# Performance work log

Measured on AMD Instinct MI355X. Metric: run time of the kernel, lower is better.

## Reference

```python
import jax, jax.numpy as jnp
import numpy as np

B, L, C, H = 2, 2048, 1024, 16
D = C // H  # dim per head

def setup_inputs() -> dict:
    key = jax.random.key(0)
    ks = jax.random.split(key, 13)
    s = 1.0 / np.sqrt(C)
    inp = {
        "query": jax.random.normal(ks[0], (B, L, C), jnp.float32),
        "key": jax.random.normal(ks[1], (B, L, C), jnp.float32),
        "value": jax.random.normal(ks[2], (B, L, C), jnp.float32),
        "mask": jax.random.randint(ks[3], (B, 1, L, L), 0, 2, jnp.int32),
        "WQ": jax.random.normal(ks[4], (C, C), jnp.float32) * s,
        "bQ": jnp.zeros((C,), jnp.float32),
        "WK": jax.random.normal(ks[5], (C, C), jnp.float32) * s,
        "bK": jnp.zeros((C,), jnp.float32),
        "WV": jax.random.normal(ks[6], (C, C), jnp.float32) * s,
        "bV": jnp.zeros((C,), jnp.float32),
        "WO": jax.random.normal(ks[7], (C, C), jnp.float32) * s,
        "bO": jnp.zeros((C,), jnp.float32),
    }
    return inp

def reference(query, key, value, mask, WQ, bQ, WK, bK, WV, bV, WO, bO):
    b = query.shape[0]
    # projections: x @ W + b  (W stored [in, out])
    Q = query @ WQ + bQ
    K = key @ WK + bK
    V = value @ WV + bV
    # [B, L, C] -> [B, H, L, D]
    def split_heads(x):
        return x.reshape(b, -1, H, D).transpose(0, 2, 1, 3)
    Qh, Kh, Vh = split_heads(Q), split_heads(K), split_heads(V)
    scores = jnp.einsum("bhqd,bhkd->bhqk", Qh, Kh) / jnp.sqrt(jnp.float32(D))
    scores = jnp.where(mask == 0, jnp.float32(-1e9), scores)
    attn = jax.nn.softmax(scores, axis=-1)
    Z = jnp.einsum("bhqk,bhkd->bhqd", attn, Vh)  # [B, H, L, D]
    Z = Z.transpose(0, 2, 1, 3).reshape(b, Q.shape[1], C)
    return Z @ WO + bO
```

## Files before the change

kernel.cpp:

```cpp
#include <hip/hip_runtime.h>

#define BB 2
#define LL 2048
#define CC 1024
#define HH 16
#define DD 64
#define MM (BB * LL)

typedef __bf16 bf16x8 __attribute__((ext_vector_type(8)));
typedef float  f32x4  __attribute__((ext_vector_type(4)));

#define LOG2E 1.44269504088896340736f
#if defined(__has_builtin)
#if __has_builtin(__builtin_amdgcn_exp2f)
#define EXP2F(x) __builtin_amdgcn_exp2f(x)
#else
#define EXP2F(x) exp2f(x)
#endif
#else
#define EXP2F(x) exp2f(x)
#endif

__device__ __forceinline__ unsigned short f2bf(float x) {
    return __builtin_bit_cast(unsigned short, (__bf16)x);
}
__device__ __forceinline__ void split2(float x, unsigned short& hi, unsigned short& lo) {
    __bf16 h = (__bf16)x;
    hi = __builtin_bit_cast(unsigned short, h);
    lo = __builtin_bit_cast(unsigned short, (__bf16)(x - (float)h));
}

#define GLOAD_LDS16(g, l)                                                      \
    __builtin_amdgcn_global_load_lds(                                          \
        (const __attribute__((address_space(1))) void*)(g),                    \
        (__attribute__((address_space(3))) void*)(l), 16, 0, 0)

#define MFMA16(a, b, c) __builtin_amdgcn_mfma_f32_16x16x32_bf16((a), (b), (c), 0, 0, 0)

__global__ __launch_bounds__(256) void w_prep(
    const float* __restrict__ W, unsigned short* __restrict__ Whi,
    unsigned short* __restrict__ Wlo)
{
    __shared__ float T[64][65];
    const int tid = threadIdx.x;
    const int k0 = blockIdx.x * 64, n0 = blockIdx.y * 64;
    #pragma unroll
    for (int p = 0; p < 4; ++p) {
        const int idx = tid + p * 256;
        const int r = idx >> 4, c4 = idx & 15;
        float4 v = *(const float4*)&W[(size_t)(k0 + r) * CC + n0 + c4 * 4];
        T[r][c4 * 4 + 0] = v.x; T[r][c4 * 4 + 1] = v.y;
        T[r][c4 * 4 + 2] = v.z; T[r][c4 * 4 + 3] = v.w;
    }
    __syncthreads();
    #pragma unroll
    for (int p = 0; p < 16; ++p) {
        const int idx = tid + p * 256;
        const int n = idx >> 6, k = idx & 63;
        unsigned short hi, lo;
        split2(T[k][n], hi, lo);
        Whi[(size_t)(n0 + n) * CC + k0 + k] = hi;
        Wlo[(size_t)(n0 + n) * CC + k0 + k] = lo;
    }
}

__global__ __launch_bounds__(256) void x_prep(
    const float* __restrict__ X, unsigned short* __restrict__ Xhi,
    unsigned short* __restrict__ Xlo)
{
    const size_t i = (size_t)blockIdx.x * 256 + threadIdx.x;
    float4 v = *(const float4*)&X[i * 4];
    unsigned short h0, l0, h1, l1, h2, l2, h3, l3;
    split2(v.x, h0, l0); split2(v.y, h1, l1);
    split2(v.z, h2, l2); split2(v.w, h3, l3);
    ushort4 hv; hv.x = h0; hv.y = h1; hv.z = h2; hv.w = h3;
    ushort4 lv; lv.x = l0; lv.y = l1; lv.z = l2; lv.w = l3;
    *(ushort4*)&Xhi[i * 4] = hv;
    *(ushort4*)&Xlo[i * 4] = lv;
}

__global__ __launch_bounds__(256) void vt_prep(
    const float* __restrict__ Vp, unsigned short* __restrict__ Vt)
{
    __shared__ float T[64][65];
    const int tid = threadIdx.x;
    const int t = blockIdx.x, h = blockIdx.y, b = blockIdx.z;
    #pragma unroll
    for (int p = 0; p < 4; ++p) {
        const int idx = tid + p * 256;
        const int r = idx >> 4, c4 = idx & 15;
        float4 v = *(const float4*)&Vp[(size_t)(b * LL + t * 64 + r) * CC + h * DD + c4 * 4];
        T[r][c4 * 4 + 0] = v.x; T[r][c4 * 4 + 1] = v.y;
        T[r][c4 * 4 + 2] = v.z; T[r][c4 * 4 + 3] = v.w;
    }
    __syncthreads();
    unsigned short* out = Vt + (size_t)(b * HH + h) * DD * LL;
    #pragma unroll
    for (int p = 0; p < 16; ++p) {
        const int idx = tid + p * 256;
        const int d = idx >> 6, l = idx & 63;
        out[(size_t)d * LL + t * 64 + l] = f2bf(T[l][d]);
    }
}

__global__ __launch_bounds__(256) void mask_pack(
    const int* __restrict__ mask, unsigned int* __restrict__ mp)
{
    const size_t wi = (size_t)blockIdx.x * 256 + threadIdx.x;
    const int* src = mask + wi * 32;
    unsigned int v = 0;
    #pragma unroll
    for (int j = 0; j < 32; j += 4) {
        int4 m4 = *(const int4*)&src[j];
        if (m4.x != 0) v |= 1u << (j + 0);
        if (m4.y != 0) v |= 1u << (j + 1);
        if (m4.z != 0) v |= 1u << (j + 2);
        if (m4.w != 0) v |= 1u << (j + 3);
    }
    mp[wi] = v;
}

template <int MODE>
__global__ __launch_bounds__(256) void gemm_split(
    const unsigned short* __restrict__ Ahi, const unsigned short* __restrict__ Alo,
    const unsigned short* __restrict__ Bhi, const unsigned short* __restrict__ Blo,
    const float* __restrict__ bias, float scale,
    float* __restrict__ Yf,
    unsigned short* __restrict__ Yhi, unsigned short* __restrict__ Ylo)
{
    __shared__ __align__(16) unsigned short Ah[128 * 32];
    __shared__ __align__(16) unsigned short Al[128 * 32];
    __shared__ __align__(16) unsigned short Bh[128 * 32];
    __shared__ __align__(16) unsigned short Bl[128 * 32];

    const int tid  = threadIdx.x;
    const int lane = tid & 63, w = tid >> 6;
    const int wr = w >> 1, wc = w & 1;
    const int lr = lane & 15, kg = lane >> 4;
    const int row0 = blockIdx.x * 128, col0 = blockIdx.y * 128;

    f32x4 acc[4][4];
    #pragma unroll
    for (int i = 0; i < 4; ++i)
        #pragma unroll
        for (int j = 0; j < 4; ++j)
            acc[i][j] = (f32x4){0.f, 0.f, 0.f, 0.f};

    const int srow = lane >> 2;
    const int ssl  = ((lane & 3) ^ ((srow >> 1) & 3)) * 8;
    const int ko   = (kg ^ ((lr >> 1) & 3)) * 8;

    const int NT = CC / 32;
    for (int kt = 0; kt < NT; ++kt) {
        const int k0 = kt * 32;
        #pragma unroll
        for (int c = 0; c < 2; ++c) {
            const int chunk = w * 2 + c;
            const int r = chunk * 16 + srow;
            GLOAD_LDS16(Ahi + (size_t)(row0 + r) * CC + k0 + ssl, &Ah[chunk * 512]);
            GLOAD_LDS16(Alo + (size_t)(row0 + r) * CC + k0 + ssl, &Al[chunk * 512]);
            GLOAD_LDS16(Bhi + (size_t)(col0 + r) * CC + k0 + ssl, &Bh[chunk * 512]);
            GLOAD_LDS16(Blo + (size_t)(col0 + r) * CC + k0 + ssl, &Bl[chunk * 512]);
        }
        __syncthreads();

        bf16x8 ah[4], al[4], bh[4], bl[4];
        #pragma unroll
        for (int i = 0; i < 4; ++i) {
            ah[i] = *(const bf16x8*)&Ah[(wr * 64 + i * 16 + lr) * 32 + ko];
            al[i] = *(const bf16x8*)&Al[(wr * 64 + i * 16 + lr) * 32 + ko];
            bh[i] = *(const bf16x8*)&Bh[(wc * 64 + i * 16 + lr) * 32 + ko];
            bl[i] = *(const bf16x8*)&Bl[(wc * 64 + i * 16 + lr) * 32 + ko];
        }
        #pragma unroll
        for (int i = 0; i < 4; ++i)
            #pragma unroll
            for (int j = 0; j < 4; ++j) {
                acc[i][j] = MFMA16(ah[i], bh[j], acc[i][j]);
                acc[i][j] = MFMA16(ah[i], bl[j], acc[i][j]);
                acc[i][j] = MFMA16(al[i], bh[j], acc[i][j]);
            }
        __syncthreads();
    }

    #pragma unroll
    for (int j = 0; j < 4; ++j) {
        const int n = col0 + wc * 64 + j * 16 + lr;
        const float bv = bias[n];
        #pragma unroll
        for (int i = 0; i < 4; ++i) {
            const int mbase = row0 + wr * 64 + i * 16 + kg * 4;
            #pragma unroll
            for (int r = 0; r < 4; ++r) {
                const float v = (acc[i][j][r] + bv) * scale;
                const int m = mbase + r;
                if (MODE == 0) {
                    Yf[(size_t)m * CC + n] = v;
                } else {
                    const int bb = m >> 11, ll = m & (LL - 1);
                    const int hh = n >> 6, dd = n & 63;
                    const size_t o = ((size_t)(bb * HH + hh) * LL + ll) * DD + dd;
                    unsigned short hi, lo;
                    split2(v, hi, lo);
                    Yhi[o] = hi; Ylo[o] = lo;
                }
            }
        }
    }
}

__global__ __launch_bounds__(256) void flash_mfma(
    const unsigned short* __restrict__ Qhi, const unsigned short* __restrict__ Qlo,
    const unsigned short* __restrict__ Khi, const unsigned short* __restrict__ Klo,
    const unsigned short* __restrict__ Vt,  const unsigned int* __restrict__ maskp,
    unsigned short* __restrict__ Zhi, unsigned short* __restrict__ Zlo)
{
    __shared__ __align__(16) unsigned short Kh_s[64 * 64];
    __shared__ __align__(16) unsigned short Kl_s[64 * 64];
    __shared__ __align__(16) unsigned short Vt_s[64 * 64];
    __shared__ __align__(16) __bf16 Ps[4][16 * 72];

    const int tid  = threadIdx.x;
    const int lane = tid & 63, w = tid >> 6;
    const int lr = lane & 15, kg = lane >> 4;
    const int q0 = blockIdx.x * 64;
    const int h = blockIdx.y, b = blockIdx.z;
    const size_t bh = (size_t)(b * HH + h);

    const unsigned short* Qhi_b = Qhi + bh * LL * DD;
    const unsigned short* Qlo_b = Qlo + bh * LL * DD;
    const unsigned short* Khi_b = Khi + bh * LL * DD;
    const unsigned short* Klo_b = Klo + bh * LL * DD;
    const unsigned short* Vt_b  = Vt  + bh * DD * LL;

    const int qrow = q0 + w * 16 + lr;
    bf16x8 qh[2], ql[2];
    #pragma unroll
    for (int s = 0; s < 2; ++s) {
        qh[s] = *(const bf16x8*)&Qhi_b[(size_t)qrow * DD + s * 32 + kg * 8];
        ql[s] = *(const bf16x8*)&Qlo_b[(size_t)qrow * DD + s * 32 + kg * 8];
    }

    f32x4 oacc[4];
    float m_r[4], l_r[4];
    #pragma unroll
    for (int r = 0; r < 4; ++r) {
        oacc[r] = (f32x4){0.f, 0.f, 0.f, 0.f};
        m_r[r] = -3.0e38f; l_r[r] = 0.f;
    }

    const int NT = LL / 64;
    for (int kt = 0; kt < NT; ++kt) {
        #pragma unroll
        for (int c = 0; c < 2; ++c) {
            const int chunk = w * 2 + c;
            const int rowi = chunk * 8 + (lane >> 3);
            const int cb   = (lane & 7) * 16;
            const int scb  = cb ^ ((rowi & 7) << 4);
            GLOAD_LDS16(Khi_b + (size_t)(kt * 64 + rowi) * DD + scb / 2, &Kh_s[chunk * 512]);
            GLOAD_LDS16(Klo_b + (size_t)(kt * 64 + rowi) * DD + scb / 2, &Kl_s[chunk * 512]);
            GLOAD_LDS16(Vt_b + (size_t)rowi * LL + kt * 64 + scb / 2,    &Vt_s[chunk * 512]);
        }
        __syncthreads();

        f32x4 sacc[4];
        #pragma unroll
        for (int j = 0; j < 4; ++j) sacc[j] = (f32x4){0.f, 0.f, 0.f, 0.f};
        __builtin_amdgcn_s_setprio(1);
        #pragma unroll
        for (int j = 0; j < 4; ++j) {
            const int krow = j * 16 + lr;
            const int rswz = (krow & 7) << 4;
            #pragma unroll
            for (int s = 0; s < 2; ++s) {
                const int cb = (s * 64 + kg * 16) ^ rswz;
                bf16x8 kh = *(const bf16x8*)((const char*)&Kh_s[0] + krow * 128 + cb);
                bf16x8 kl = *(const bf16x8*)((const char*)&Kl_s[0] + krow * 128 + cb);
                sacc[j] = MFMA16(qh[s], kh, sacc[j]);
                sacc[j] = MFMA16(qh[s], kl, sacc[j]);
                sacc[j] = MFMA16(ql[s], kh, sacc[j]);
            }
        }
        __builtin_amdgcn_s_setprio(0);

        float mxr[4];
        #pragma unroll
        for (int r = 0; r < 4; ++r) {
            const int qr = q0 + w * 16 + kg * 4 + r;
            const unsigned int* mb = maskp + ((size_t)b * LL + qr) * (LL / 32) + kt * 2;
            const unsigned int m0 = mb[0], m1 = mb[1];
            float mx = -3.0e38f;
            #pragma unroll
            for (int j = 0; j < 4; ++j) {
                const unsigned int wsel = (j < 2) ? m0 : m1;
                const int bit = (j & 1) * 16 + lr;
                if (((wsel >> bit) & 1u) == 0u) sacc[j][r] = -1.0e9f;
                mx = fmaxf(mx, sacc[j][r]);
            }
            #pragma unroll
            for (int off = 1; off < 16; off <<= 1)
                mx = fmaxf(mx, __shfl_xor(mx, off, 16));
            mxr[r] = mx;
        }

        const float g = fmaxf(fmaxf(mxr[0] - m_r[0], mxr[1] - m_r[1]),
                              fmaxf(mxr[2] - m_r[2], mxr[3] - m_r[3]));
        if (!__all(g <= 8.0f)) {
            #pragma unroll
            for (int r = 0; r < 4; ++r) {
                const float mnew = fmaxf(m_r[r], mxr[r]);
                const float f = EXP2F(m_r[r] - mnew);
                m_r[r] = mnew;
                l_r[r] *= f;
                #pragma unroll
                for (int jd = 0; jd < 4; ++jd) oacc[jd][r] *= f;
            }
        }

        #pragma unroll
        for (int r = 0; r < 4; ++r) {
            float sum = 0.f;
            #pragma unroll
            for (int j = 0; j < 4; ++j) {
                const float p = EXP2F(sacc[j][r] - m_r[r]);
                sum += p;
                Ps[w][(kg * 4 + r) * 72 + j * 16 + lr] = (__bf16)p;
            }
            #pragma unroll
            for (int off = 1; off < 16; off <<= 1)
                sum += __shfl_xor(sum, off, 16);
            l_r[r] += sum;
        }

        __builtin_amdgcn_s_setprio(1);
        #pragma unroll
        for (int s = 0; s < 2; ++s) {
            bf16x8 pa = *(const bf16x8*)&Ps[w][lr * 72 + s * 32 + kg * 8];
            #pragma unroll
            for (int jd = 0; jd < 4; ++jd) {
                const int vrow = jd * 16 + lr;
                const int cb = (s * 64 + kg * 16) ^ ((vrow & 7) << 4);
                bf16x8 vb = *(const bf16x8*)((const char*)&Vt_s[0] + vrow * 128 + cb);
                oacc[jd] = MFMA16(pa, vb, oacc[jd]);
            }
        }
        __builtin_amdgcn_s_setprio(0);
        __syncthreads();
    }

    #pragma unroll
    for (int r = 0; r < 4; ++r) {
        const float inv = 1.0f / l_r[r];
        const int qg = q0 + w * 16 + kg * 4 + r;
        const size_t rowb = ((size_t)(b * LL + qg)) * CC + h * DD;
        #pragma unroll
        for (int jd = 0; jd < 4; ++jd) {
            unsigned short hi, lo;
            split2(oacc[jd][r] * inv, hi, lo);
            Zhi[rowb + jd * 16 + lr] = hi;
            Zlo[rowb + jd * 16 + lr] = lo;
        }
    }
}

extern "C" void kernel_launch(void* const* d_in, const int* in_sizes, int n_in,
                              void* d_out, int out_size, void* d_ws, size_t ws_size,
                              hipStream_t stream)
{
    const float* query = (const float*)d_in[0];
    const float* key   = (const float*)d_in[1];
    const float* value = (const float*)d_in[2];
    const int*   mask  = (const int*)d_in[3];
    const float* WQ = (const float*)d_in[4];
    const float* bQ = (const float*)d_in[5];
    const float* WK = (const float*)d_in[6];
    const float* bK = (const float*)d_in[7];
    const float* WV = (const float*)d_in[8];
    const float* bV = (const float*)d_in[9];
    const float* WO = (const float*)d_in[10];
    const float* bO = (const float*)d_in[11];
    float* out = (float*)d_out;

    char* ws = (char*)d_ws;
    const size_t MB = 1024 * 1024;
    unsigned short* WQt_hi = (unsigned short*)(ws + 0 * MB);
    unsigned short* WQt_lo = (unsigned short*)(ws + 2 * MB);
    unsigned short* WKt_hi = (unsigned short*)(ws + 4 * MB);
    unsigned short* WKt_lo = (unsigned short*)(ws + 6 * MB);
    unsigned short* WVt_hi = (unsigned short*)(ws + 8 * MB);
    unsigned short* WVt_lo = (unsigned short*)(ws + 10 * MB);
    unsigned short* WOt_hi = (unsigned short*)(ws + 12 * MB);
    unsigned short* WOt_lo = (unsigned short*)(ws + 14 * MB);
    unsigned short* Xhi    = (unsigned short*)(ws + 16 * MB);
    unsigned short* Xlo    = (unsigned short*)(ws + 24 * MB);
    unsigned short* Qh_hi  = (unsigned short*)(ws + 32 * MB);
    unsigned short* Qh_lo  = (unsigned short*)(ws + 40 * MB);
    unsigned short* Kh_hi  = (unsigned short*)(ws + 48 * MB);
    unsigned short* Kh_lo  = (unsigned short*)(ws + 56 * MB);
    float*          Vp     = (float*)(ws + 64 * MB);
    unsigned short* Vt     = (unsigned short*)(ws + 80 * MB);
    unsigned int*   maskp  = (unsigned int*)(ws + 88 * MB);

    const dim3 blk(256);
    const dim3 wgrid(CC / 64, CC / 64);
    w_prep<<<wgrid, blk, 0, stream>>>(WQ, WQt_hi, WQt_lo);
    w_prep<<<wgrid, blk, 0, stream>>>(WK, WKt_hi, WKt_lo);
    w_prep<<<wgrid, blk, 0, stream>>>(WV, WVt_hi, WVt_lo);
    w_prep<<<wgrid, blk, 0, stream>>>(WO, WOt_hi, WOt_lo);
    mask_pack<<<dim3((BB * LL * (LL / 32)) / 256), blk, 0, stream>>>(mask, maskp);

    const dim3 ggrid(MM / 128, CC / 128);
    const dim3 xgrid((size_t)MM * CC / 4 / 256);

    x_prep<<<xgrid, blk, 0, stream>>>(query, Xhi, Xlo);
    gemm_split<1><<<ggrid, blk, 0, stream>>>(Xhi, Xlo, WQt_hi, WQt_lo, bQ,
                                             0.125f * LOG2E, nullptr, Qh_hi, Qh_lo);
    x_prep<<<xgrid, blk, 0, stream>>>(key, Xhi, Xlo);
    gemm_split<1><<<ggrid, blk, 0, stream>>>(Xhi, Xlo, WKt_hi, WKt_lo, bK, 1.0f,
                                             nullptr, Kh_hi, Kh_lo);
    x_prep<<<xgrid, blk, 0, stream>>>(value, Xhi, Xlo);
    gemm_split<0><<<ggrid, blk, 0, stream>>>(Xhi, Xlo, WVt_hi, WVt_lo, bV, 1.0f,
                                             Vp, nullptr, nullptr);
    vt_prep<<<dim3(LL / 64, HH, BB), blk, 0, stream>>>(Vp, Vt);

    flash_mfma<<<dim3(LL / 64, HH, BB), blk, 0, stream>>>(
        Qh_hi, Qh_lo, Kh_hi, Kh_lo, Vt, maskp, Xhi, Xlo);

    gemm_split<0><<<ggrid, blk, 0, stream>>>(Xhi, Xlo, WOt_hi, WOt_lo, bO, 1.0f,
                                             out, nullptr, nullptr);
}
```

Before: 483.9 us.

## Batch QKV projections into one launch and write transposed V directly

Merges the four weight-prep launches and the three input-split launches into single launches that pick their source from the grid z/y index. Q, K and V projections become one GEMM over a 3x-tall grid whose epilogue picks weights, bias and output layout per block, and V is written straight as transposed bf16, so the fp32 V buffer and the vt_prep pass go away. The output projection gets its own GEMM with 64-row tiles, which doubles the block count. This cuts launch overhead, raises occupancy for the smaller GEMMs and drops one round trip through memory. The cost is more workspace and scattered transposed stores of V from the GEMM epilogue.

After: 423.0 us. -12.6%, faster.

```diff
diff --git a/kernel.cpp b/kernel.cpp
--- a/kernel.cpp
+++ b/kernel.cpp
@@ -37,13 +37,19 @@
 
 #define MFMA16(a, b, c) __builtin_amdgcn_mfma_f32_16x16x32_bf16((a), (b), (c), 0, 0, 0)
 
-__global__ __launch_bounds__(256) void w_prep(
-    const float* __restrict__ W, unsigned short* __restrict__ Whi,
-    unsigned short* __restrict__ Wlo)
+__global__ __launch_bounds__(256) void w_prep4(
+    const float* __restrict__ WQ, const float* __restrict__ WK,
+    const float* __restrict__ WV, const float* __restrict__ WO,
+    char* __restrict__ wsbase)
 {
     __shared__ float T[64][65];
     const int tid = threadIdx.x;
     const int k0 = blockIdx.x * 64, n0 = blockIdx.y * 64;
+    const int z = blockIdx.z;
+    const float* W = (z == 0) ? WQ : (z == 1) ? WK : (z == 2) ? WV : WO;
+    unsigned short* Whi = (unsigned short*)(wsbase + (size_t)z * 4 * 1024 * 1024);
+    unsigned short* Wlo = Whi + (size_t)CC * CC;
+
     #pragma unroll
     for (int p = 0; p < 4; ++p) {
         const int idx = tid + p * 256;
@@ -64,43 +70,23 @@
     }
 }
 
-__global__ __launch_bounds__(256) void x_prep(
-    const float* __restrict__ X, unsigned short* __restrict__ Xhi,
-    unsigned short* __restrict__ Xlo)
-{
+__global__ __launch_bounds__(256) void x_prep3(
+    const float* __restrict__ query, const float* __restrict__ key,
+    const float* __restrict__ value,
+    unsigned short* __restrict__ Xhi, unsigned short* __restrict__ Xlo)
+{
+    const int y = blockIdx.y;
+    const float* src = (y == 0) ? query : (y == 1) ? key : value;
     const size_t i = (size_t)blockIdx.x * 256 + threadIdx.x;
-    float4 v = *(const float4*)&X[i * 4];
+    const size_t o = (size_t)y * MM * CC + i * 4;
+    float4 v = *(const float4*)&src[i * 4];
     unsigned short h0, l0, h1, l1, h2, l2, h3, l3;
     split2(v.x, h0, l0); split2(v.y, h1, l1);
     split2(v.z, h2, l2); split2(v.w, h3, l3);
     ushort4 hv; hv.x = h0; hv.y = h1; hv.z = h2; hv.w = h3;
     ushort4 lv; lv.x = l0; lv.y = l1; lv.z = l2; lv.w = l3;
-    *(ushort4*)&Xhi[i * 4] = hv;
-    *(ushort4*)&Xlo[i * 4] = lv;
-}
-
-__global__ __launch_bounds__(256) void vt_prep(
-    const float* __restrict__ Vp, unsigned short* __restrict__ Vt)
-{
-    __shared__ float T[64][65];
-    const int tid = threadIdx.x;
-    const int t = blockIdx.x, h = blockIdx.y, b = blockIdx.z;
-    #pragma unroll
-    for (int p = 0; p < 4; ++p) {
-        const int idx = tid + p * 256;
-        const int r = idx >> 4, c4 = idx & 15;
-        float4 v = *(const float4*)&Vp[(size_t)(b * LL + t * 64 + r) * CC + h * DD + c4 * 4];
-        T[r][c4 * 4 + 0] = v.x; T[r][c4 * 4 + 1] = v.y;
-        T[r][c4 * 4 + 2] = v.z; T[r][c4 * 4 + 3] = v.w;
-    }
-    __syncthreads();
-    unsigned short* out = Vt + (size_t)(b * HH + h) * DD * LL;
-    #pragma unroll
-    for (int p = 0; p < 16; ++p) {
-        const int idx = tid + p * 256;
-        const int d = idx >> 6, l = idx & 63;
-        out[(size_t)d * LL + t * 64 + l] = f2bf(T[l][d]);
-    }
+    *(ushort4*)&Xhi[o] = hv;
+    *(ushort4*)&Xlo[o] = lv;
 }
 
 __global__ __launch_bounds__(256) void mask_pack(
@@ -120,13 +106,15 @@
     mp[wi] = v;
 }
 
-template <int MODE>
-__global__ __launch_bounds__(256) void gemm_split(
+__global__ __launch_bounds__(256) void qkv_gemm(
     const unsigned short* __restrict__ Ahi, const unsigned short* __restrict__ Alo,
-    const unsigned short* __restrict__ Bhi, const unsigned short* __restrict__ Blo,
-    const float* __restrict__ bias, float scale,
-    float* __restrict__ Yf,
-    unsigned short* __restrict__ Yhi, unsigned short* __restrict__ Ylo)
+    const unsigned short* __restrict__ WQt_hi, const unsigned short* __restrict__ WKt_hi,
+    const unsigned short* __restrict__ WVt_hi,
+    const float* __restrict__ bQ, const float* __restrict__ bK,
+    const float* __restrict__ bV,
+    unsigned short* __restrict__ Qhi, unsigned short* __restrict__ Qlo,
+    unsigned short* __restrict__ Khi, unsigned short* __restrict__ Klo,
+    unsigned short* __restrict__ Vt)
 {
     __shared__ __align__(16) unsigned short Ah[128 * 32];
     __shared__ __align__(16) unsigned short Al[128 * 32];
@@ -137,7 +125,15 @@
     const int lane = tid & 63, w = tid >> 6;
     const int wr = w >> 1, wc = w & 1;
     const int lr = lane & 15, kg = lane >> 4;
-    const int row0 = blockIdx.x * 128, col0 = blockIdx.y * 128;
+    const int row0 = blockIdx.x * 128;
+    const int col0 = blockIdx.y * 128;
+    const int sel  = row0 >> 12;
+
+    const unsigned short* Bhi =
+        (sel == 0) ? WQt_hi : (sel == 1) ? WKt_hi : WVt_hi;
+    const unsigned short* Blo = Bhi + (size_t)CC * CC;
+    const float* bias = (sel == 0) ? bQ : (sel == 1) ? bK : bV;
+    const float scale = (sel == 0) ? 0.125f * LOG2E : 1.0f;
 
     f32x4 acc[4][4];
     #pragma unroll
@@ -187,24 +183,105 @@
     for (int j = 0; j < 4; ++j) {
         const int n = col0 + wc * 64 + j * 16 + lr;
         const float bv = bias[n];
+        const int hh = n >> 6, dd = n & 63;
         #pragma unroll
         for (int i = 0; i < 4; ++i) {
             const int mbase = row0 + wr * 64 + i * 16 + kg * 4;
             #pragma unroll
             for (int r = 0; r < 4; ++r) {
                 const float v = (acc[i][j][r] + bv) * scale;
-                const int m = mbase + r;
-                if (MODE == 0) {
-                    Yf[(size_t)m * CC + n] = v;
+                const int ml = (mbase + r) & (MM - 1);
+                const int bb = ml >> 11, ll = ml & (LL - 1);
+                if (sel == 2) {
+                    Vt[((size_t)(bb * HH + hh) * DD + dd) * LL + ll] = f2bf(v);
                 } else {
-                    const int bb = m >> 11, ll = m & (LL - 1);
-                    const int hh = n >> 6, dd = n & 63;
                     const size_t o = ((size_t)(bb * HH + hh) * LL + ll) * DD + dd;
                     unsigned short hi, lo;
                     split2(v, hi, lo);
-                    Yhi[o] = hi; Ylo[o] = lo;
+                    if (sel == 0) { Qhi[o] = hi; Qlo[o] = lo; }
+                    else          { Khi[o] = hi; Klo[o] = lo; }
                 }
             }
+        }
+    }
+}
+
+__global__ __launch_bounds__(256) void o_gemm(
+    const unsigned short* __restrict__ Ahi, const unsigned short* __restrict__ Alo,
+    const unsigned short* __restrict__ Bhi, const unsigned short* __restrict__ Blo,
+    const float* __restrict__ bias, float* __restrict__ Yf)
+{
+    __shared__ __align__(16) unsigned short Ah[64 * 32];
+    __shared__ __align__(16) unsigned short Al[64 * 32];
+    __shared__ __align__(16) unsigned short Bh[128 * 32];
+    __shared__ __align__(16) unsigned short Bl[128 * 32];
+
+    const int tid  = threadIdx.x;
+    const int lane = tid & 63, w = tid >> 6;
+    const int wr = w >> 1, wc = w & 1;
+    const int lr = lane & 15, kg = lane >> 4;
+    const int row0 = blockIdx.x * 64, col0 = blockIdx.y * 128;
+
+    f32x4 acc[2][4];
+    #pragma unroll
+    for (int i = 0; i < 2; ++i)
+        #pragma unroll
+        for (int j = 0; j < 4; ++j)
+            acc[i][j] = (f32x4){0.f, 0.f, 0.f, 0.f};
+
+    const int srow = lane >> 2;
+    const int ssl  = ((lane & 3) ^ ((srow >> 1) & 3)) * 8;
+    const int ko   = (kg ^ ((lr >> 1) & 3)) * 8;
+
+    const int NT = CC / 32;
+    for (int kt = 0; kt < NT; ++kt) {
+        const int k0 = kt * 32;
+        {
+            const int r = w * 16 + srow;
+            GLOAD_LDS16(Ahi + (size_t)(row0 + r) * CC + k0 + ssl, &Ah[w * 512]);
+            GLOAD_LDS16(Alo + (size_t)(row0 + r) * CC + k0 + ssl, &Al[w * 512]);
+        }
+        #pragma unroll
+        for (int c = 0; c < 2; ++c) {
+            const int chunk = w * 2 + c;
+            const int r = chunk * 16 + srow;
+            GLOAD_LDS16(Bhi + (size_t)(col0 + r) * CC + k0 + ssl, &Bh[chunk * 512]);
+            GLOAD_LDS16(Blo + (size_t)(col0 + r) * CC + k0 + ssl, &Bl[chunk * 512]);
+        }
+        __syncthreads();
+
+        bf16x8 ah[2], al[2], bh[4], bl[4];
+        #pragma unroll
+        for (int i = 0; i < 2; ++i) {
+            ah[i] = *(const bf16x8*)&Ah[(wr * 32 + i * 16 + lr) * 32 + ko];
+            al[i] = *(const bf16x8*)&Al[(wr * 32 + i * 16 + lr) * 32 + ko];
+        }
+        #pragma unroll
+        for (int j = 0; j < 4; ++j) {
+            bh[j] = *(const bf16x8*)&Bh[(wc * 64 + j * 16 + lr) * 32 + ko];
+            bl[j] = *(const bf16x8*)&Bl[(wc * 64 + j * 16 + lr) * 32 + ko];
+        }
+        #pragma unroll
+        for (int i = 0; i < 2; ++i)
+            #pragma unroll
+            for (int j = 0; j < 4; ++j) {
+                acc[i][j] = MFMA16(ah[i], bh[j], acc[i][j]);
+                acc[i][j] = MFMA16(ah[i], bl[j], acc[i][j]);
+                acc[i][j] = MFMA16(al[i], bh[j], acc[i][j]);
+            }
+        __syncthreads();
+    }
+
+    #pragma unroll
+    for (int j = 0; j < 4; ++j) {
+        const int n = col0 + wc * 64 + j * 16 + lr;
+        const float bv = bias[n];
+        #pragma unroll
+        for (int i = 0; i < 2; ++i) {
+            const int mbase = row0 + wr * 32 + i * 16 + kg * 4;
+            #pragma unroll
+            for (int r = 0; r < 4; ++r)
+                Yf[(size_t)(mbase + r) * CC + n] = acc[i][j][r] + bv;
         }
     }
 }
@@ -384,48 +461,34 @@
     char* ws = (char*)d_ws;
     const size_t MB = 1024 * 1024;
     unsigned short* WQt_hi = (unsigned short*)(ws + 0 * MB);
-    unsigned short* WQt_lo = (unsigned short*)(ws + 2 * MB);
     unsigned short* WKt_hi = (unsigned short*)(ws + 4 * MB);
-    unsigned short* WKt_lo = (unsigned short*)(ws + 6 * MB);
     unsigned short* WVt_hi = (unsigned short*)(ws + 8 * MB);
-    unsigned short* WVt_lo = (unsigned short*)(ws + 10 * MB);
     unsigned short* WOt_hi = (unsigned short*)(ws + 12 * MB);
     unsigned short* WOt_lo = (unsigned short*)(ws + 14 * MB);
-    unsigned short* Xhi    = (unsigned short*)(ws + 16 * MB);
-    unsigned short* Xlo    = (unsigned short*)(ws + 24 * MB);
-    unsigned short* Qh_hi  = (unsigned short*)(ws + 32 * MB);
-    unsigned short* Qh_lo  = (unsigned short*)(ws + 40 * MB);
-    unsigned short* Kh_hi  = (unsigned short*)(ws + 48 * MB);
-    unsigned short* Kh_lo  = (unsigned short*)(ws + 56 * MB);
-    float*          Vp     = (float*)(ws + 64 * MB);
-    unsigned short* Vt     = (unsigned short*)(ws + 80 * MB);
-    unsigned int*   maskp  = (unsigned int*)(ws + 88 * MB);
+    unsigned short* Xall_hi = (unsigned short*)(ws + 16 * MB);
+    unsigned short* Xall_lo = (unsigned short*)(ws + 40 * MB);
+    unsigned short* Qh_hi  = (unsigned short*)(ws + 64 * MB);
+    unsigned short* Qh_lo  = (unsigned short*)(ws + 72 * MB);
+    unsigned short* Kh_hi  = (unsigned short*)(ws + 80 * MB);
+    unsigned short* Kh_lo  = (unsigned short*)(ws + 88 * MB);
+    unsigned short* Vt     = (unsigned short*)(ws + 96 * MB);
+    unsigned int*   maskp  = (unsigned int*)(ws + 104 * MB);
+    unsigned short* Zh_hi  = (unsigned short*)(ws + 16 * MB);
+    unsigned short* Zh_lo  = (unsigned short*)(ws + 24 * MB);
 
     const dim3 blk(256);
-    const dim3 wgrid(CC / 64, CC / 64);
-    w_prep<<<wgrid, blk, 0, stream>>>(WQ, WQt_hi, WQt_lo);
-    w_prep<<<wgrid, blk, 0, stream>>>(WK, WKt_hi, WKt_lo);
-    w_prep<<<wgrid, blk, 0, stream>>>(WV, WVt_hi, WVt_lo);
-    w_prep<<<wgrid, blk, 0, stream>>>(WO, WOt_hi, WOt_lo);
+    w_prep4<<<dim3(CC / 64, CC / 64, 4), blk, 0, stream>>>(WQ, WK, WV, WO, ws);
     mask_pack<<<dim3((BB * LL * (LL / 32)) / 256), blk, 0, stream>>>(mask, maskp);
-
-    const dim3 ggrid(MM / 128, CC / 128);
-    const dim3 xgrid((size_t)MM * CC / 4 / 256);
-
-    x_prep<<<xgrid, blk, 0, stream>>>(query, Xhi, Xlo);
-    gemm_split<1><<<ggrid, blk, 0, stream>>>(Xhi, Xlo, WQt_hi, WQt_lo, bQ,
-                                             0.125f * LOG2E, nullptr, Qh_hi, Qh_lo);
-    x_prep<<<xgrid, blk, 0, stream>>>(key, Xhi, Xlo);
-    gemm_split<1><<<ggrid, blk, 0, stream>>>(Xhi, Xlo, WKt_hi, WKt_lo, bK, 1.0f,
-                                             nullptr, Kh_hi, Kh_lo);
-    x_prep<<<xgrid, blk, 0, stream>>>(value, Xhi, Xlo);
-    gemm_split<0><<<ggrid, blk, 0, stream>>>(Xhi, Xlo, WVt_hi, WVt_lo, bV, 1.0f,
-                                             Vp, nullptr, nullptr);
-    vt_prep<<<dim3(LL / 64, HH, BB), blk, 0, stream>>>(Vp, Vt);
+    x_prep3<<<dim3((size_t)MM * CC / 4 / 256, 3), blk, 0, stream>>>(
+        query, key, value, Xall_hi, Xall_lo);
+
+    qkv_gemm<<<dim3(3 * MM / 128, CC / 128), blk, 0, stream>>>(
+        Xall_hi, Xall_lo, WQt_hi, WKt_hi, WVt_hi, bQ, bK, bV,
+        Qh_hi, Qh_lo, Kh_hi, Kh_lo, Vt);
 
     flash_mfma<<<dim3(LL / 64, HH, BB), blk, 0, stream>>>(
-        Qh_hi, Qh_lo, Kh_hi, Kh_lo, Vt, maskp, Xhi, Xlo);
-
-    gemm_split<0><<<ggrid, blk, 0, stream>>>(Xhi, Xlo, WOt_hi, WOt_lo, bO, 1.0f,
-                                             out, nullptr, nullptr);
-}
+        Qh_hi, Qh_lo, Kh_hi, Kh_lo, Vt, maskp, Zh_hi, Zh_lo);
+
+    o_gemm<<<dim3(MM / 64, CC / 128), blk, 0, stream>>>(
+        Zh_hi, Zh_lo, WOt_hi, WOt_lo, bO, out);
+}
```
